# Optimization experiments

Hardware: AMD Instinct MI355X
Metric: run time of the kernel (lower is better)

The kernel has to match this reference:

```python
import jax, jax.numpy as jnp
import numpy as np

IN_C = 256
N_E = 8192
E_DIM = 256
BETA = 0.25
K = 3
LN_EPS = 1e-5


def _conv(x, w, b):
    # x: [B,C,H,W], w: [O,I,K,K]
    y = jax.lax.conv_general_dilated(
        x, w, window_strides=(1, 1), padding='SAME',
        dimension_numbers=('NCHW', 'OIHW', 'NCHW'))
    return y + b[None, :, None, None]


def _layernorm(x, g, b):
    mu = jnp.mean(x, axis=-1, keepdims=True)
    var = jnp.var(x, axis=-1, keepdims=True)
    return (x - mu) * jax.lax.rsqrt(var + LN_EPS) * g + b


def setup_inputs() -> dict:
    key = jax.random.key(0)
    ks = jax.random.split(key, 8)
    fan_emb = IN_C * K * K
    fan_unemb = E_DIM * K * K
    return {
        'z': jax.random.normal(ks[0], (16, IN_C, 32, 32), dtype=jnp.float32),
        'emb_w': jax.random.normal(ks[1], (E_DIM, IN_C, K, K), dtype=jnp.float32) / np.sqrt(fan_emb),
        'emb_b': jnp.zeros((E_DIM,), dtype=jnp.float32),
        'ln_g': jnp.ones((E_DIM,), dtype=jnp.float32),
        'ln_b': jnp.zeros((E_DIM,), dtype=jnp.float32),
        'codebook': jax.random.uniform(ks[2], (N_E, E_DIM), dtype=jnp.float32,
                                       minval=-1.0 / N_E, maxval=1.0 / N_E),
        'unemb_w': jax.random.normal(ks[3], (IN_C, E_DIM, K, K), dtype=jnp.float32) / np.sqrt(fan_unemb),
        'unemb_b': jnp.zeros((IN_C,), dtype=jnp.float32),
    }


def reference(z, emb_w, emb_b, ln_g, ln_b, codebook, unemb_w, unemb_b):
    B, _, H, W = z.shape
    # emb conv, then b c h w -> b h w c
    ze = _conv(z, emb_w, emb_b)                       # [B,E,H,W]
    ze = jnp.transpose(ze, (0, 2, 3, 1))              # [B,H,W,E]
    zf = _layernorm(ze.reshape(B, H * W, E_DIM), ln_g, ln_b)
    zf = zf.reshape(-1, E_DIM)                        # [B*H*W, E]
    # squared distances: ||z||^2 + ||e||^2 - 2 z e^T
    d = (jnp.sum(zf ** 2, axis=1, keepdims=True)
         + jnp.sum(codebook ** 2, axis=1)[None, :]
         - 2.0 * jnp.einsum('bd,nd->bn', zf, codebook))  # [B*H*W, N_E]
    idx = jnp.argmin(d, axis=1)                       # [B*H*W]
    z_q = codebook[idx].reshape(ze.shape)             # [B,H,W,E]
    # legacy loss
    loss = (jnp.mean((jax.lax.stop_gradient(z_q) - ze) ** 2)
            + BETA * jnp.mean((z_q - jax.lax.stop_gradient(ze)) ** 2))
    # straight-through
    z_q = ze + jax.lax.stop_gradient(z_q - ze)
    z_q = jnp.transpose(z_q, (0, 3, 1, 2))            # [B,E,H,W]
    out = _conv(z_q, unemb_w, unemb_b)                # [B,C,H,W]
    return out, loss, idx
```

## Files before the change

kernel.cpp:

```cpp
#include <hip/hip_runtime.h>
#include <hip/hip_bf16.h>

#define B_SZ 16
#define CIN 256
#define EDIM 256
#define NE 8192
#define HW 32
#define NPIX (B_SZ*HW*HW)
#define OUT_ELEMS (B_SZ*CIN*HW*HW)
#define SCREEN_T 3.2e-4f
#define CAND_SLOTS 128

typedef __attribute__((ext_vector_type(8))) short short8;
typedef __attribute__((ext_vector_type(4))) short short4v;
typedef __attribute__((ext_vector_type(4))) float f32x4;

__device__ __forceinline__ float block_sum(float v, float* sbuf) {
    #pragma unroll
    for (int off = 32; off > 0; off >>= 1) v += __shfl_down(v, off, 64);
    int wid = threadIdx.x >> 6;
    int lane = threadIdx.x & 63;
    if (lane == 0) sbuf[wid] = v;
    __syncthreads();
    if (threadIdx.x == 0) sbuf[0] = sbuf[0] + sbuf[1] + sbuf[2] + sbuf[3];
    __syncthreads();
    float r = sbuf[0];
    __syncthreads();
    return r;
}

__device__ __forceinline__ double wave_sum_d(double v) {
    #pragma unroll
    for (int off = 32; off > 0; off >>= 1) v += __shfl_down(v, off, 64);
    return __shfl(v, 0, 64);
}

__device__ __forceinline__ unsigned short bf16rne(float f) {
    unsigned int u = __float_as_uint(f);
    unsigned int r = (u + 0x7FFFu + ((u >> 16) & 1u)) >> 16;
    return (unsigned short)r;
}
__device__ __forceinline__ float bf2f(unsigned short h) {
    return __uint_as_float((unsigned int)h << 16);
}

__device__ __forceinline__ unsigned int mapU(float f) {
    unsigned int u = __float_as_uint(f);
    return (u & 0x80000000u) ? ~u : (u | 0x80000000u);
}
__device__ __forceinline__ float unmapU(unsigned int m) {
    unsigned int u = (m & 0x80000000u) ? (m ^ 0x80000000u) : ~m;
    return __uint_as_float(u);
}

__global__ void prep_kernel(const float* __restrict__ emb_w, unsigned short* __restrict__ w1bh,
                            unsigned short* __restrict__ w1bl,
                            const float* __restrict__ unemb_w, unsigned short* __restrict__ w2hi,
                            unsigned short* __restrict__ w2lo, const float* __restrict__ cb,
                            unsigned short* __restrict__ cbhi, unsigned short* __restrict__ cblo) {
    int blk = blockIdx.x;
    if (blk < 2304) {
        int e = blk / 9, tap = blk % 9;
        int c = threadIdx.x;
        float v = emb_w[(size_t)e * 2304 + c * 9 + tap];
        unsigned short h = bf16rne(v);
        unsigned short l = bf16rne(v - bf2f(h));
        size_t j = (size_t)e * 2304 + tap * 256 + c;
        w1bh[j] = h; w1bl[j] = l;
    } else if (blk < 4608) {
        int b2 = blk - 2304;
        int cout = b2 / 9, tap = b2 % 9;
        int e = threadIdx.x;
        float v = unemb_w[(size_t)cout * 2304 + e * 9 + tap];
        unsigned short h = bf16rne(v);
        unsigned short l = bf16rne(v - bf2f(h));
        size_t j = (size_t)cout * 2304 + tap * 256 + e;
        w2hi[j] = h; w2lo[j] = l;
    } else {
        int i = (blk - 4608) * 256 + threadIdx.x;
        size_t base = (size_t)i * 4;
        float4 v = *(const float4*)(cb + base);
        short4v sh, sl;
        unsigned short h;
        h = bf16rne(v.x); sh[0] = (short)h; sl[0] = (short)bf16rne(v.x - bf2f(h));
        h = bf16rne(v.y); sh[1] = (short)h; sl[1] = (short)bf16rne(v.y - bf2f(h));
        h = bf16rne(v.z); sh[2] = (short)h; sl[2] = (short)bf16rne(v.z - bf2f(h));
        h = bf16rne(v.w); sh[3] = (short)h; sl[3] = (short)bf16rne(v.w - bf2f(h));
        *(short4v*)(cbhi + base) = sh;
        *(short4v*)(cblo + base) = sl;
    }
}

#define EM_REG 6528
__global__ __launch_bounds__(256, 4) void conv_emb_mfma(const float* __restrict__ z,
                                                        const unsigned short* __restrict__ w1bh,
                                                        const unsigned short* __restrict__ w1bl,
                                                        float* __restrict__ ze) {
    __shared__ char smem[3 * EM_REG];
    const int tid = threadIdx.x;
    const int wid = tid >> 6, lane = tid & 63;
    const int l15 = lane & 15, lg = lane >> 4;
    const int bh = blockIdx.x;
    const int b = bh >> 5, h = bh & 31;
    const int ch = blockIdx.y;

    for (int i = tid; i < (3 * EM_REG) / 16; i += 256) ((int4*)smem)[i] = make_int4(0, 0, 0, 0);

    const f32x4 zero4 = {0.f, 0.f, 0.f, 0.f};
    f32x4 acc[2][2];
    acc[0][0] = zero4; acc[0][1] = zero4; acc[1][0] = zero4; acc[1][1] = zero4;

    for (int cc = 0; cc < 256; cc += 32) {
        __syncthreads();
        #pragma unroll
        for (int rd = 0; rd < 2; ++rd) {
            int t2 = rd * 256 + tid;
            if (t2 < 408) {
                int row = t2 >> 2;
                int oct = t2 & 3;
                int r = row / 34, wp = row - r * 34;
                int hh = h + r - 1;
                if (hh >= 0 && hh < 32 && wp >= 1 && wp <= 32) {
                    const float* zp = z + (size_t)b * 262144 + (size_t)(cc + oct * 8) * 1024
                                    + hh * 32 + (wp - 1);
                    short8 vh, vm, vl;
                    #pragma unroll
                    for (int j = 0; j < 8; ++j) {
                        float v = zp[(size_t)j * 1024];
                        unsigned short h1 = bf16rne(v);
                        float rm = v - bf2f(h1);
                        unsigned short m1 = bf16rne(rm);
                        float rl = rm - bf2f(m1);
                        unsigned short l1 = bf16rne(rl);
                        vh[j] = (short)h1; vm[j] = (short)m1; vl[j] = (short)l1;
                    }
                    int boff = row * 64 + ((oct * 16) ^ ((wp & 3) << 4));
                    *(short8*)(smem + boff) = vh;
                    *(short8*)(smem + EM_REG + boff) = vm;
                    *(short8*)(smem + 2 * EM_REG + boff) = vl;
                }
            }
        }
        __syncthreads();

        #pragma unroll
        for (int tap = 0; tap < 9; ++tap) {
            const int r = tap / 3, kw = tap % 3;
            short8 a1[2], a2[2], a3[2], bhf[2], blf[2];
            #pragma unroll
            for (int mf = 0; mf < 2; ++mf) {
                int wpr = mf * 16 + l15 + kw;
                int boff = (r * 34 + wpr) * 64 + ((lg * 16) ^ ((wpr & 3) << 4));
                a1[mf] = *(const short8*)(smem + boff);
                a2[mf] = *(const short8*)(smem + EM_REG + boff);
                a3[mf] = *(const short8*)(smem + 2 * EM_REG + boff);
            }
            #pragma unroll
            for (int nf = 0; nf < 2; ++nf) {
                int e_idx = (ch << 7) + (wid << 5) + (nf << 4) + l15;
                size_t goff = (size_t)e_idx * 2304 + tap * 256 + cc + lg * 8;
                bhf[nf] = *(const short8*)(w1bh + goff);
                blf[nf] = *(const short8*)(w1bl + goff);
            }
            #pragma unroll
            for (int mf = 0; mf < 2; ++mf)
                #pragma unroll
                for (int nf = 0; nf < 2; ++nf) {
                    acc[mf][nf] = __builtin_amdgcn_mfma_f32_16x16x32_bf16(a1[mf], bhf[nf], acc[mf][nf], 0, 0, 0);
                    acc[mf][nf] = __builtin_amdgcn_mfma_f32_16x16x32_bf16(a1[mf], blf[nf], acc[mf][nf], 0, 0, 0);
                    acc[mf][nf] = __builtin_amdgcn_mfma_f32_16x16x32_bf16(a2[mf], bhf[nf], acc[mf][nf], 0, 0, 0);
                    acc[mf][nf] = __builtin_amdgcn_mfma_f32_16x16x32_bf16(a2[mf], blf[nf], acc[mf][nf], 0, 0, 0);
                    acc[mf][nf] = __builtin_amdgcn_mfma_f32_16x16x32_bf16(a3[mf], bhf[nf], acc[mf][nf], 0, 0, 0);
                }
        }
    }

    int p0 = (b * 32 + h) * 32;
    #pragma unroll
    for (int mf = 0; mf < 2; ++mf)
        #pragma unroll
        for (int nf = 0; nf < 2; ++nf) {
            int e_idx = (ch << 7) + (wid << 5) + (nf << 4) + l15;
            #pragma unroll
            for (int rr = 0; rr < 4; ++rr) {
                int pix = mf * 16 + lg * 4 + rr;
                ze[(size_t)(p0 + pix) * 256 + e_idx] = acc[mf][nf][rr];
            }
        }
}

__global__ __launch_bounds__(256) void ln_kernel(float* __restrict__ ze, const float* __restrict__ bias,
                                                 const float* __restrict__ g,
                                                 const float* __restrict__ bta,
                                                 unsigned short* __restrict__ zfb,
                                                 float* __restrict__ snorm, float* __restrict__ mu_a,
                                                 float* __restrict__ r_a) {
    int wid = threadIdx.x >> 6, lane = threadIdx.x & 63;
    int p = blockIdx.x * 4 + wid;
    float* zp = ze + (size_t)p * 256;
    float x0 = zp[lane]       + bias[lane];
    float x1 = zp[lane + 64]  + bias[lane + 64];
    float x2 = zp[lane + 128] + bias[lane + 128];
    float x3 = zp[lane + 192] + bias[lane + 192];
    zp[lane] = x0; zp[lane + 64] = x1; zp[lane + 128] = x2; zp[lane + 192] = x3;
    double lsum = (((double)x0 + (double)x1) + (double)x2) + (double)x3;
    double sum = wave_sum_d(lsum);
    float mu = ((float)sum) / 256.0f;
    float e0 = x0 - mu, e1 = x1 - mu, e2 = x2 - mu, e3 = x3 - mu;
    double lsq = (((double)(e0 * e0) + (double)(e1 * e1)) + (double)(e2 * e2)) + (double)(e3 * e3);
    double vs = wave_sum_d(lsq);
    float var = ((float)vs) / 256.0f;
    float r = 1.0f / sqrtf(var + 1e-5f);
    float y0 = ((e0 * r) * g[lane])       + bta[lane];
    float y1 = ((e1 * r) * g[lane + 64])  + bta[lane + 64];
    float y2 = ((e2 * r) * g[lane + 128]) + bta[lane + 128];
    float y3 = ((e3 * r) * g[lane + 192]) + bta[lane + 192];
    unsigned short* zq = zfb + (size_t)p * 256;
    zq[lane] = bf16rne(y0); zq[lane + 64] = bf16rne(y1);
    zq[lane + 128] = bf16rne(y2); zq[lane + 192] = bf16rne(y3);
    double lys = (((double)(y0 * y0) + (double)(y1 * y1)) + (double)(y2 * y2)) + (double)(y3 * y3);
    double ss = wave_sum_d(lys);
    if (lane == 0) { snorm[p] = (float)ss; mu_a[p] = mu; r_a[p] = r; }
}

__global__ __launch_bounds__(512) void screen_kernel(const unsigned short* __restrict__ zf_bf,
                                                     const unsigned short* __restrict__ cb_bf,
                                                     int* __restrict__ ccnt,
                                                     int* __restrict__ cand) {
    __shared__ unsigned int smax[64];
    __shared__ int scnt[64];
    __shared__ int sbuf[64][CAND_SLOTS];
    const int tid = threadIdx.x;
    const int w = tid >> 6;
    const int lane = tid & 63;
    const int l15 = lane & 15, lg = lane >> 4;
    const int p0 = blockIdx.x * 64;
    const int rowoff = w * 16 + l15;
    const int lg8 = lg * 8;

    if (tid < 64) { smax[tid] = 0u; scnt[tid] = 0; }
    __syncthreads();

    short8 aF[4][8];
    #pragma unroll
    for (int mf = 0; mf < 4; ++mf)
        #pragma unroll
        for (int ks = 0; ks < 8; ++ks)
            aF[mf][ks] = *reinterpret_cast<const short8*>(
                zf_bf + (size_t)(p0 + mf * 16 + l15) * 256 + ks * 32 + lg8);

    const f32x4 zero4 = {0.f, 0.f, 0.f, 0.f};
    float runL[4][4], runS[4][4];
    #pragma unroll
    for (int mf = 0; mf < 4; ++mf)
        #pragma unroll
        for (int r = 0; r < 4; ++r) { runL[mf][r] = -3.4e38f; runS[mf][r] = -3.4e38f; }

    for (int c = 0; c < 8; ++c) {
        const int nrow = c * 128 + rowoff;
        const unsigned short* bp = cb_bf + (size_t)nrow * 256 + lg8;
        short8 bF[8];
        #pragma unroll
        for (int ks = 0; ks < 8; ++ks) bF[ks] = *reinterpret_cast<const short8*>(bp + ks * 32);
        f32x4 acc[4] = {zero4, zero4, zero4, zero4};
        #pragma unroll
        for (int ks = 0; ks < 8; ++ks)
            #pragma unroll
            for (int mf = 0; mf < 4; ++mf)
                acc[mf] = __builtin_amdgcn_mfma_f32_16x16x32_bf16(aF[mf][ks], bF[ks], acc[mf], 0, 0, 0);
        #pragma unroll
        for (int mf = 0; mf < 4; ++mf)
            #pragma unroll
            for (int r = 0; r < 4; ++r) runL[mf][r] = fmaxf(runL[mf][r], acc[mf][r]);
    }
    #pragma unroll
    for (int mf = 0; mf < 4; ++mf)
        #pragma unroll
        for (int r = 0; r < 4; ++r) {
            float v = runL[mf][r];
            v = fmaxf(v, __shfl_xor(v, 1, 64));
            v = fmaxf(v, __shfl_xor(v, 2, 64));
            v = fmaxf(v, __shfl_xor(v, 4, 64));
            v = fmaxf(v, __shfl_xor(v, 8, 64));
            runL[mf][r] = v;
            if (l15 == 0) atomicMax(&smax[mf * 16 + lg * 4 + r], mapU(v));
        }
    __syncthreads();
    #pragma unroll
    for (int mf = 0; mf < 4; ++mf)
        #pragma unroll
        for (int r = 0; r < 4; ++r) runS[mf][r] = unmapU(smax[mf * 16 + lg * 4 + r]);

    for (int c = 0; c < 64; ++c) {
        const int nrow = c * 128 + rowoff;
        const unsigned short* bp = cb_bf + (size_t)nrow * 256 + lg8;
        short8 bF[8];
        #pragma unroll
        for (int ks = 0; ks < 8; ++ks) bF[ks] = *reinterpret_cast<const short8*>(bp + ks * 32);
        f32x4 acc[4] = {zero4, zero4, zero4, zero4};
        #pragma unroll
        for (int ks = 0; ks < 8; ++ks)
            #pragma unroll
            for (int mf = 0; mf < 4; ++mf)
                acc[mf] = __builtin_amdgcn_mfma_f32_16x16x32_bf16(aF[mf][ks], bF[ks], acc[mf], 0, 0, 0);

        unsigned qual = 0u;
        #pragma unroll
        for (int mf = 0; mf < 4; ++mf)
            #pragma unroll
            for (int r = 0; r < 4; ++r) {
                float dd = acc[mf][r];
                if (dd >= fmaxf(runS[mf][r], runL[mf][r]) - SCREEN_T) qual |= (1u << (mf * 4 + r));
                runL[mf][r] = fmaxf(runL[mf][r], dd);
            }
        if (qual) {
            #pragma unroll
            for (int mf = 0; mf < 4; ++mf)
                #pragma unroll
                for (int r = 0; r < 4; ++r)
                    if (qual & (1u << (mf * 4 + r))) {
                        int pix = mf * 16 + lg * 4 + r;
                        int s = atomicAdd(&scnt[pix], 1);
                        if (s < CAND_SLOTS) sbuf[pix][s] = nrow;
                    }
        }
        if ((c & 7) == 7) {
            #pragma unroll
            for (int mf = 0; mf < 4; ++mf)
                #pragma unroll
                for (int r = 0; r < 4; ++r) {
                    float v = runL[mf][r];
                    v = fmaxf(v, __shfl_xor(v, 1, 64));
                    v = fmaxf(v, __shfl_xor(v, 2, 64));
                    v = fmaxf(v, __shfl_xor(v, 4, 64));
                    v = fmaxf(v, __shfl_xor(v, 8, 64));
                    runL[mf][r] = v;
                    if (l15 == 0) atomicMax(&smax[mf * 16 + lg * 4 + r], mapU(v));
                }
            #pragma unroll
            for (int mf = 0; mf < 4; ++mf)
                #pragma unroll
                for (int r = 0; r < 4; ++r) runS[mf][r] = unmapU(smax[mf * 16 + lg * 4 + r]);
        }
    }
    __syncthreads();
    if (tid < 64) ccnt[p0 + tid] = (scnt[tid] < CAND_SLOTS) ? scnt[tid] : CAND_SLOTS;
    for (int i = tid; i < 64 * CAND_SLOTS; i += 512) {
        int pix = i >> 7;
        int s = i & (CAND_SLOTS - 1);
        if (s < scnt[pix] && s < CAND_SLOTS)
            cand[(size_t)(p0 + pix) * CAND_SLOTS + s] = sbuf[pix][s];
    }
}

__global__ __launch_bounds__(256) void rescore_kernel(const float* __restrict__ ze,
                                                      const float* __restrict__ mu_a,
                                                      const float* __restrict__ r_a,
                                                      const float* __restrict__ snorm,
                                                      const float* __restrict__ g,
                                                      const float* __restrict__ bta,
                                                      const float* __restrict__ cb,
                                                      const int* __restrict__ ccnt,
                                                      const int* __restrict__ cand,
                                                      int* __restrict__ idx_i,
                                                      float* __restrict__ idx_f) {
    int p = blockIdx.x * 4 + (threadIdx.x >> 6);
    int lane = threadIdx.x & 63;
    int cnt = ccnt[p];
    if (cnt > CAND_SLOTS) cnt = CAND_SLOTS;
    float d = 3.4e38f;
    int ix = 0x7FFFFFFF;
    float mu = mu_a[p];
    float r = r_a[p];
    float sz = snorm[p];
    const float* zr = ze + (size_t)p * 256;
    for (int s = lane; s < cnt; s += 64) {
        int n = cand[(size_t)p * CAND_SLOTS + s];
        const float* cr = cb + (size_t)n * 256;
        float a0 = 0.f, a1 = 0.f, a2 = 0.f, a3 = 0.f;
        for (int k0 = 0; k0 < 256; k0 += 4) {
            float4 zq = *(const float4*)(zr + k0);
            float4 gq = *(const float4*)(g + k0);
            float4 bq = *(const float4*)(bta + k0);
            float4 cq = *(const float4*)(cr + k0);
            float d0 = zq.x - mu; float y0 = ((d0 * r) * gq.x) + bq.x;
            float d1 = zq.y - mu; float y1 = ((d1 * r) * gq.y) + bq.y;
            float d2 = zq.z - mu; float y2 = ((d2 * r) * gq.z) + bq.z;
            float d3 = zq.w - mu; float y3 = ((d3 * r) * gq.w) + bq.w;
            a0 = fmaf(y0, cq.x, a0);
            a1 = fmaf(y1, cq.y, a1);
            a2 = fmaf(y2, cq.z, a2);
            a3 = fmaf(y3, cq.w, a3);
        }
        float dot32 = (float)(((double)a0 + (double)a1) + ((double)a2 + (double)a3));
        float dd = fmaf(-2.0f, dot32, sz);
        if (dd < d || (dd == d && n < ix)) { d = dd; ix = n; }
    }
    #pragma unroll
    for (int off = 32; off > 0; off >>= 1) {
        float ov = __shfl_down(d, off, 64);
        int   oi = __shfl_down(ix, off, 64);
        if (ov < d || (ov == d && oi < ix)) { d = ov; ix = oi; }
    }
    if (lane == 0) {
        idx_i[p] = ix;
        idx_f[p] = (float)ix;
    }
}

__global__ void loss_partial_kernel(const float* __restrict__ ze, const float* __restrict__ cb,
                                    const int* __restrict__ idx, float* __restrict__ partials) {
    __shared__ float sbuf[4];
    float sum = 0.f;
    const int total = NPIX * 256;
    for (int i = blockIdx.x * blockDim.x + threadIdx.x; i < total; i += gridDim.x * blockDim.x) {
        int p = i >> 8;
        int e = i & 255;
        float d = cb[(size_t)idx[p] * 256 + e] - ze[i];
        sum = fmaf(d, d, sum);
    }
    sum = block_sum(sum, sbuf);
    if (threadIdx.x == 0) partials[blockIdx.x] = sum;
}

__global__ void loss_final_kernel(const float* __restrict__ partials, float* __restrict__ loss_out) {
    __shared__ float sbuf[4];
    float v = partials[threadIdx.x];
    v = block_sum(v, sbuf);
    if (threadIdx.x == 0) *loss_out = v * (1.25f / (float)(NPIX * 256));
}

#define AROWB 128
#define ALO   13056
__global__ __launch_bounds__(256, 4) void conv_unemb_mfma(const unsigned short* __restrict__ cb_hi,
                                                          const unsigned short* __restrict__ cb_lo,
                                                          const int* __restrict__ idx,
                                                          const unsigned short* __restrict__ w2_hi,
                                                          const unsigned short* __restrict__ w2_lo,
                                                          const float* __restrict__ bias,
                                                          float* __restrict__ out) {
    __shared__ char smem[2 * ALO];
    float* ot = (float*)smem;
    const int tid = threadIdx.x;
    const int wid = tid >> 6, lane = tid & 63;
    const int l15 = lane & 15, lg = lane >> 4;
    const int bh = blockIdx.x;
    const int b = bh >> 5, h = bh & 31;
    const int ch = blockIdx.y;

    for (int i = tid; i < (2 * ALO) / 16; i += 256) ((int4*)smem)[i] = make_int4(0, 0, 0, 0);

    int nrow[3], rok[3], wpos[3], rr3[3];
    #pragma unroll
    for (int rd = 0; rd < 3; ++rd) {
        int t2 = rd * 256 + tid;
        int row = t2 >> 3;
        int r = row >> 5, w = row & 31;
        int hh = h + r - 1;
        rok[rd] = (hh >= 0 && hh < 32) ? 1 : 0;
        rr3[rd] = r; wpos[rd] = w;
        nrow[rd] = rok[rd] ? idx[(b * 32 + hh) * 32 + w] : 0;
    }
    __syncthreads();

    const f32x4 zero4 = {0.f, 0.f, 0.f, 0.f};
    f32x4 acc[2][2];
    acc[0][0] = zero4; acc[0][1] = zero4; acc[1][0] = zero4; acc[1][1] = zero4;

    for (int ec = 0; ec < 4; ++ec) {
        if (ec) __syncthreads();
        #pragma unroll
        for (int rd = 0; rd < 3; ++rd) {
            if (rok[rd]) {
                int t2 = rd * 256 + tid;
                int eo = (t2 & 7) * 8;
                size_t gsrc = (size_t)nrow[rd] * 256 + ec * 64 + eo;
                short8 vh = *(const short8*)(cb_hi + gsrc);
                short8 vl = *(const short8*)(cb_lo + gsrc);
                int wp = wpos[rd] + 1;
                int rowbase = (rr3[rd] * 34 + wp) * AROWB;
                int boff = (eo * 2) ^ ((wp & 7) << 4);
                *(short8*)(smem + rowbase + boff) = vh;
                *(short8*)(smem + ALO + rowbase + boff) = vl;
            }
        }
        __syncthreads();

        #pragma unroll
        for (int tap = 0; tap < 9; ++tap) {
            const int r = tap / 3, kw = tap % 3;
            #pragma unroll
            for (int ks = 0; ks < 2; ++ks) {
                int e2 = ks * 32 + lg * 8;
                short8 ah[2], al[2], bh2[2], bl2[2];
                #pragma unroll
                for (int mf = 0; mf < 2; ++mf) {
                    int wp = mf * 16 + l15 + kw;
                    int rowbase = (r * 34 + wp) * AROWB;
                    int boff = (e2 * 2) ^ ((wp & 7) << 4);
                    ah[mf] = *(const short8*)(smem + rowbase + boff);
                    al[mf] = *(const short8*)(smem + ALO + rowbase + boff);
                }
                #pragma unroll
                for (int nf = 0; nf < 2; ++nf) {
                    int cout = (ch << 7) + (wid << 5) + (nf << 4) + l15;
                    size_t goff = (size_t)cout * 2304 + tap * 256 + ec * 64 + e2;
                    bh2[nf] = *(const short8*)(w2_hi + goff);
                    bl2[nf] = *(const short8*)(w2_lo + goff);
                }
                #pragma unroll
                for (int mf = 0; mf < 2; ++mf)
                    #pragma unroll
                    for (int nf = 0; nf < 2; ++nf) {
                        acc[mf][nf] = __builtin_amdgcn_mfma_f32_16x16x32_bf16(ah[mf], bh2[nf], acc[mf][nf], 0, 0, 0);
                        acc[mf][nf] = __builtin_amdgcn_mfma_f32_16x16x32_bf16(ah[mf], bl2[nf], acc[mf][nf], 0, 0, 0);
                        acc[mf][nf] = __builtin_amdgcn_mfma_f32_16x16x32_bf16(al[mf], bh2[nf], acc[mf][nf], 0, 0, 0);
                    }
            }
        }
    }
    __syncthreads();
    #pragma unroll
    for (int mf = 0; mf < 2; ++mf)
        #pragma unroll
        for (int nf = 0; nf < 2; ++nf) {
            int cl = (wid << 5) + (nf << 4) + l15;
            #pragma unroll
            for (int rr = 0; rr < 4; ++rr) {
                int px = mf * 16 + lg * 4 + rr;
                ot[cl * 36 + px] = acc[mf][nf][rr];
            }
        }
    __syncthreads();
    int row = tid >> 1, half = tid & 1;
    int cout = (ch << 7) + row;
    float bv = bias[cout];
    float* dst = out + ((size_t)(b * 256 + cout) * 32 + h) * 32 + half * 16;
    const float* src = ot + row * 36 + half * 16;
    #pragma unroll
    for (int q = 0; q < 4; ++q) {
        float4 v = *(const float4*)(src + q * 4);
        v.x += bv; v.y += bv; v.z += bv; v.w += bv;
        *(float4*)(dst + q * 4) = v;
    }
}

extern "C" void kernel_launch(void* const* d_in, const int* in_sizes, int n_in,
                              void* d_out, int out_size, void* d_ws, size_t ws_size,
                              hipStream_t stream) {
    const float* z       = (const float*)d_in[0];
    const float* emb_w   = (const float*)d_in[1];
    const float* emb_b   = (const float*)d_in[2];
    const float* ln_g    = (const float*)d_in[3];
    const float* ln_b    = (const float*)d_in[4];
    const float* cb      = (const float*)d_in[5];
    const float* unemb_w = (const float*)d_in[6];
    const float* unemb_b = (const float*)d_in[7];

    float* out    = (float*)d_out;
    float* lossp  = out + OUT_ELEMS;
    float* idxf   = out + OUT_ELEMS + 1;

    float* ws = (float*)d_ws;
    float* ze_t = ws;
    unsigned short* zf_bf = (unsigned short*)(ze_t + (size_t)NPIX * 256);
    unsigned short* cb_hi = (unsigned short*)((float*)zf_bf + 2097152);
    unsigned short* cb_lo = (unsigned short*)((float*)cb_hi + 1048576);
    float* snorm = (float*)cb_lo + 1048576;
    float* mu_a  = snorm + NPIX;
    float* r_a   = mu_a + NPIX;
    unsigned short* w1bh = (unsigned short*)(r_a + NPIX);
    unsigned short* w1bl = (unsigned short*)((float*)w1bh + 294912);
    unsigned short* w2_hi = (unsigned short*)((float*)w1bl + 294912);
    unsigned short* w2_lo = (unsigned short*)((float*)w2_hi + 294912);
    int*   ccnt  = (int*)((float*)w2_lo + 294912);
    int*   cand  = ccnt + NPIX;
    int*   idxi  = cand + (size_t)NPIX * CAND_SLOTS;
    float* partials = (float*)(idxi + NPIX);

    hipLaunchKernelGGL(prep_kernel, dim3(6656), dim3(256), 0, stream,
                       emb_w, w1bh, w1bl, unemb_w, w2_hi, w2_lo, cb, cb_hi, cb_lo);
    hipLaunchKernelGGL(conv_emb_mfma, dim3(512, 2), dim3(256), 0, stream, z, w1bh, w1bl, ze_t);
    hipLaunchKernelGGL(ln_kernel, dim3(NPIX / 4), dim3(256), 0, stream, ze_t, emb_b, ln_g, ln_b,
                       zf_bf, snorm, mu_a, r_a);
    hipLaunchKernelGGL(screen_kernel, dim3(256), dim3(512), 0, stream, zf_bf, cb_hi, ccnt, cand);
    hipLaunchKernelGGL(rescore_kernel, dim3(NPIX / 4), dim3(256), 0, stream,
                       ze_t, mu_a, r_a, snorm, ln_g, ln_b, cb, ccnt, cand, idxi, idxf);
    hipLaunchKernelGGL(loss_partial_kernel, dim3(256), dim3(256), 0, stream, ze_t, cb, idxi, partials);
    hipLaunchKernelGGL(loss_final_kernel, dim3(1), dim3(256), 0, stream, partials, lossp);
    hipLaunchKernelGGL(conv_unemb_mfma, dim3(512, 2), dim3(256), 0, stream,
                       cb_hi, cb_lo, idxi, w2_hi, w2_lo, unemb_b, out);
}
```

Before: 575.1 us.

## Split codebook screening across two blocks per pixel tile and double-buffer B loads

The screening kernel now launches a second grid dimension so each block scans half of the codebook (4096 entries) for its 64 pixels. This doubles the block count from 256 to 512, which lets the grid fill more CUs. Each half keeps its own candidate list of 64 slots, and the rescore kernel merges the two lists. The main loop also prefetches the next codebook fragment into registers while the current one is computed. In exchange, each half builds its running max threshold from only half the codebook, so more candidates may pass the screen, overflow is now capped at 64 per half, and register pressure goes up.

```diff
diff --git a/kernel.cpp b/kernel.cpp
--- a/kernel.cpp
+++ b/kernel.cpp
@@ -9,7 +9,7 @@
 #define NPIX (B_SZ*HW*HW)
 #define OUT_ELEMS (B_SZ*CIN*HW*HW)
 #define SCREEN_T 3.2e-4f
-#define CAND_SLOTS 128
+#define CAND_H 64
 
 typedef __attribute__((ext_vector_type(8))) short short8;
 typedef __attribute__((ext_vector_type(4))) short short4v;
@@ -229,12 +229,14 @@
                                                      int* __restrict__ cand) {
     __shared__ unsigned int smax[64];
     __shared__ int scnt[64];
-    __shared__ int sbuf[64][CAND_SLOTS];
+    __shared__ int sbuf[64][CAND_H];
     const int tid = threadIdx.x;
     const int w = tid >> 6;
     const int lane = tid & 63;
     const int l15 = lane & 15, lg = lane >> 4;
     const int p0 = blockIdx.x * 64;
+    const int nh = blockIdx.y;
+    const int nbase = nh << 12;
     const int rowoff = w * 16 + l15;
     const int lg8 = lg * 8;
 
@@ -256,9 +258,10 @@
         #pragma unroll
         for (int r = 0; r < 4; ++r) { runL[mf][r] = -3.4e38f; runS[mf][r] = -3.4e38f; }
 
-    for (int c = 0; c < 8; ++c) {
-        const int nrow = c * 128 + rowoff;
-        const unsigned short* bp = cb_bf + (size_t)nrow * 256 + lg8;
+    const unsigned short* basep = cb_bf + (size_t)(nbase + rowoff) * 256 + lg8;
+
+    for (int c = 0; c < 4; ++c) {
+        const unsigned short* bp = basep + (size_t)c * 128 * 256;
         short8 bF[8];
         #pragma unroll
         for (int ks = 0; ks < 8; ++ks) bF[ks] = *reinterpret_cast<const short8*>(bp + ks * 32);
@@ -291,19 +294,18 @@
         #pragma unroll
         for (int r = 0; r < 4; ++r) runS[mf][r] = unmapU(smax[mf * 16 + lg * 4 + r]);
 
-    for (int c = 0; c < 64; ++c) {
-        const int nrow = c * 128 + rowoff;
-        const unsigned short* bp = cb_bf + (size_t)nrow * 256 + lg8;
-        short8 bF[8];
-        #pragma unroll
-        for (int ks = 0; ks < 8; ++ks) bF[ks] = *reinterpret_cast<const short8*>(bp + ks * 32);
+    short8 bA[8], bB[8];
+    #pragma unroll
+    for (int ks = 0; ks < 8; ++ks) bA[ks] = *reinterpret_cast<const short8*>(basep + ks * 32);
+
+    auto compute = [&](const short8* bF, int c) {
+        const int nrow = nbase + c * 128 + rowoff;
         f32x4 acc[4] = {zero4, zero4, zero4, zero4};
         #pragma unroll
         for (int ks = 0; ks < 8; ++ks)
             #pragma unroll
             for (int mf = 0; mf < 4; ++mf)
                 acc[mf] = __builtin_amdgcn_mfma_f32_16x16x32_bf16(aF[mf][ks], bF[ks], acc[mf], 0, 0, 0);
-
         unsigned qual = 0u;
         #pragma unroll
         for (int mf = 0; mf < 4; ++mf)
@@ -321,7 +323,7 @@
                     if (qual & (1u << (mf * 4 + r))) {
                         int pix = mf * 16 + lg * 4 + r;
                         int s = atomicAdd(&scnt[pix], 1);
-                        if (s < CAND_SLOTS) sbuf[pix][s] = nrow;
+                        if (s < CAND_H) sbuf[pix][s] = nrow;
                     }
         }
         if ((c & 7) == 7) {
@@ -342,14 +344,34 @@
                 #pragma unroll
                 for (int r = 0; r < 4; ++r) runS[mf][r] = unmapU(smax[mf * 16 + lg * 4 + r]);
         }
-    }
-    __syncthreads();
-    if (tid < 64) ccnt[p0 + tid] = (scnt[tid] < CAND_SLOTS) ? scnt[tid] : CAND_SLOTS;
-    for (int i = tid; i < 64 * CAND_SLOTS; i += 512) {
-        int pix = i >> 7;
-        int s = i & (CAND_SLOTS - 1);
-        if (s < scnt[pix] && s < CAND_SLOTS)
-            cand[(size_t)(p0 + pix) * CAND_SLOTS + s] = sbuf[pix][s];
+    };
+
+    for (int c = 0; c < 32; c += 2) {
+        {
+            const unsigned short* np = basep + (size_t)(c + 1) * 128 * 256;
+            #pragma unroll
+            for (int ks = 0; ks < 8; ++ks) bB[ks] = *reinterpret_cast<const short8*>(np + ks * 32);
+            compute(bA, c);
+        }
+        {
+            if (c + 2 < 32) {
+                const unsigned short* np = basep + (size_t)(c + 2) * 128 * 256;
+                #pragma unroll
+                for (int ks = 0; ks < 8; ++ks) bA[ks] = *reinterpret_cast<const short8*>(np + ks * 32);
+            }
+            compute(bB, c + 1);
+        }
+    }
+    __syncthreads();
+    if (tid < 64) {
+        int v = scnt[tid];
+        ccnt[nh * NPIX + p0 + tid] = (v < CAND_H) ? v : CAND_H;
+    }
+    for (int i = tid; i < 64 * CAND_H; i += 512) {
+        int pix = i >> 6;
+        int s = i & (CAND_H - 1);
+        if (s < scnt[pix])
+            cand[(size_t)(p0 + pix) * 128 + nh * CAND_H + s] = sbuf[pix][s];
     }
 }
 
@@ -366,16 +388,18 @@
                                                       float* __restrict__ idx_f) {
     int p = blockIdx.x * 4 + (threadIdx.x >> 6);
     int lane = threadIdx.x & 63;
-    int cnt = ccnt[p];
-    if (cnt > CAND_SLOTS) cnt = CAND_SLOTS;
+    int cnt0 = ccnt[p];           if (cnt0 > CAND_H) cnt0 = CAND_H;
+    int cnt1 = ccnt[NPIX + p];    if (cnt1 > CAND_H) cnt1 = CAND_H;
+    int total = cnt0 + cnt1;
     float d = 3.4e38f;
     int ix = 0x7FFFFFFF;
     float mu = mu_a[p];
     float r = r_a[p];
     float sz = snorm[p];
     const float* zr = ze + (size_t)p * 256;
-    for (int s = lane; s < cnt; s += 64) {
-        int n = cand[(size_t)p * CAND_SLOTS + s];
+    for (int s = lane; s < total; s += 64) {
+        int n = (s < cnt0) ? cand[(size_t)p * 128 + s]
+                           : cand[(size_t)p * 128 + CAND_H + (s - cnt0)];
         const float* cr = cb + (size_t)n * 256;
         float a0 = 0.f, a1 = 0.f, a2 = 0.f, a3 = 0.f;
         for (int k0 = 0; k0 < 256; k0 += 4) {
@@ -574,8 +598,8 @@
     unsigned short* w2_hi = (unsigned short*)((float*)w1bl + 294912);
     unsigned short* w2_lo = (unsigned short*)((float*)w2_hi + 294912);
     int*   ccnt  = (int*)((float*)w2_lo + 294912);
-    int*   cand  = ccnt + NPIX;
-    int*   idxi  = cand + (size_t)NPIX * CAND_SLOTS;
+    int*   cand  = ccnt + 2 * NPIX;
+    int*   idxi  = cand + (size_t)NPIX * 128;
     float* partials = (float*)(idxi + NPIX);
 
     hipLaunchKernelGGL(prep_kernel, dim3(6656), dim3(256), 0, stream,
@@ -583,7 +607,7 @@
     hipLaunchKernelGGL(conv_emb_mfma, dim3(512, 2), dim3(256), 0, stream, z, w1bh, w1bl, ze_t);
     hipLaunchKernelGGL(ln_kernel, dim3(NPIX / 4), dim3(256), 0, stream, ze_t, emb_b, ln_g, ln_b,
                        zf_bf, snorm, mu_a, r_a);
-    hipLaunchKernelGGL(screen_kernel, dim3(256), dim3(512), 0, stream, zf_bf, cb_hi, ccnt, cand);
+    hipLaunchKernelGGL(screen_kernel, dim3(256, 2), dim3(512), 0, stream, zf_bf, cb_hi, ccnt, cand);
     hipLaunchKernelGGL(rescore_kernel, dim3(NPIX / 4), dim3(256), 0, stream,
                        ze_t, mu_a, r_a, snorm, ln_g, ln_b, cb, ccnt, cand, idxi, idxf);
     hipLaunchKernelGGL(loss_partial_kernel, dim3(256), dim3(256), 0, stream, ze_t, cb, idxi, partials);
```

Measured after the change: 672.6 us. 17.0% more time.
